# Kernel optimization log

Measured on AMD Instinct MI355X. Metric: run time of the kernel, lower is better.

## Reference

```python
import jax, jax.numpy as jnp
import numpy as np

BS, NP, H, L = 4, 1000, 128, 4
RBF_DIM, EDGE_D, NODE_D, K_NEI, NKP = 20, 16, 64, 9, 12
N = BS * 2 * NP
E = N * K_NEI
STD = 10.0          # CoordNomralizer std (mean = 0)
R_CUT = 1.0
SIGMA, GAMMA = 25.0, 10.0  # protein_surface_intersection constants (EquiDock-style)


def setup_inputs():
    key = jax.random.key(0)
    keys = iter(jax.random.split(key, 64))
    def nrm(shape, scale=None):
        s = scale if scale is not None else 1.0 / np.sqrt(shape[-2] if len(shape) > 1 else shape[-1])
        return (jax.random.normal(next(keys), shape, jnp.float32) * s).astype(jnp.float32)
    rng = np.random.default_rng(0)
    # kNN-style edges: K_NEI random intra-sample neighbors per node (messages src -> dst)
    dst = np.repeat(np.arange(N), K_NEI)
    samp = dst // (2 * NP)
    src = samp * (2 * NP) + rng.integers(0, 2 * NP, size=E)
    rots = []
    for _ in range(BS):  # sample_transformation: random rotation per complex
        A = rng.normal(size=(3, 3))
        Q, Rm = np.linalg.qr(A)
        Q = Q * np.sign(np.diag(Rm))
        if np.linalg.det(Q) < 0:
            Q[:, 0] = -Q[:, 0]
        rots.append(Q)
    return dict(
        X=nrm((N, 4, 3), 1.0),
        node_attr=nrm((N, NODE_D), 1.0),
        edge_attr=nrm((E, EDGE_D), 1.0),
        center=nrm((BS, 3), 0.1),
        keypoints=nrm((BS * NKP, 3), 1.0),
        rot=jnp.asarray(np.stack(rots), jnp.float32),
        trans=jnp.asarray(rng.random((BS, 3)), jnp.float32),
        W_in1=nrm((NODE_D, H)), b_in1=jnp.zeros((H,), jnp.float32),
        W_in2=nrm((H, H)), b_in2=jnp.zeros((H,), jnp.float32),
        msg_W=nrm((L, 2 * H + RBF_DIM + EDGE_D, H)), msg_b=jnp.zeros((L, H), jnp.float32),
        upd_W1=nrm((L, 2 * H, H)), upd_b1=jnp.zeros((L, H), jnp.float32),
        upd_W2=nrm((L, H, H)), upd_b2=jnp.zeros((L, H), jnp.float32),
        x_W=nrm((L, H, H)), v_W=nrm((L, H, H)),
        att_W=nrm((L, H, H)),
        act_W1=nrm((L, H, H)), act_b1=jnp.zeros((L, H), jnp.float32),
        act_W2=nrm((L, H, H)), act_b2=jnp.zeros((L, H), jnp.float32),
        geb_Wv1=nrm((H, H)), geb_Wv2=nrm((H, H)),
        geb_W1=nrm((2 * H, H)), geb_b1=jnp.zeros((H,), jnp.float32),
        geb_W2=nrm((H, 2 * H)), geb_b2=jnp.zeros((2 * H,), jnp.float32),
        scale_W1=nrm((H + 1, H // 2)), scale_b1=jnp.zeros((H // 2,), jnp.float32),
        scale_W2=nrm((H // 2, 1)), scale_b2=jnp.ones((1,), jnp.float32),
        final_W=nrm((H, NKP)),
        src=jnp.asarray(src, jnp.int32), dst=jnp.asarray(dst, jnp.int32),
    )


def _mse(a, b):
    return jnp.mean((a - b) ** 2)


def _kabsch(Y1, Y2):
    # optimal R, t with Y1 @ R + t ~= Y2
    c1, c2 = Y1.mean(0), Y2.mean(0)
    Hm = (Y1 - c1).T @ (Y2 - c2)
    U, S, Vt = jnp.linalg.svd(Hm)
    d = jnp.sign(jnp.linalg.det(U @ Vt))
    sc = jnp.stack([jnp.ones_like(d), jnp.ones_like(d), d])
    R = U @ (Vt * sc[:, None])
    t = c2 - c1 @ R
    return R, t


def _intersect(A, B):
    # G(x) = gamma + sigma * log sum_j exp(-||x - y_j||^2 / sigma)
    d2 = jnp.sum((A[:, None, :] - B[None, :, :]) ** 2, -1)
    return GAMMA + SIGMA * jax.nn.logsumexp(-d2 / SIGMA, axis=1)


def reference(X, node_attr, edge_attr, center, keypoints, rot, trans,
              W_in1, b_in1, W_in2, b_in2, msg_W, msg_b, upd_W1, upd_b1, upd_W2, upd_b2,
              x_W, v_W, att_W, act_W1, act_b1, act_W2, act_b2,
              geb_Wv1, geb_Wv2, geb_W1, geb_b1, geb_W2, geb_b2,
              scale_W1, scale_b1, scale_W2, scale_b2, final_W, src, dst):
    silu = jax.nn.silu
    # centering (structured layout: [BS, seg(0=receptor,1=ligand), NP, 4, 3])
    Xs = X.reshape(BS, 2, NP, 4, 3) - center[:, None, None, None, :]
    kp = keypoints.reshape(BS, NKP, 3) - center[:, None, :]
    ori = Xs[:, :, :, 1, :]                       # CA coords, pre-rotation
    Xs = Xs.at[:, 0].set(jnp.einsum('bnac,bcd->bnad', Xs[:, 0], rot) + STD * trans[:, None, None, :])
    tkp = jnp.einsum('bkc,bcd->bkd', kp, rot) + STD * trans[:, None, :]
    Xs, ori, kp, tkp = Xs / STD, ori / STD, kp / STD, tkp / STD
    Xca = Xs[:, :, :, 1, :].reshape(N, 3)

    h = silu(node_attr @ W_in1 + b_in1) @ W_in2 + b_in2
    v = jnp.zeros((N, H, 3), h.dtype)
    diff = Xca[dst] - Xca[src]
    norm = jnp.sqrt(jnp.sum(diff ** 2, -1)) + 1e-8
    dirv = diff / norm[:, None]
    nvec = jnp.arange(1, RBF_DIM + 1, dtype=h.dtype)
    rbf = jnp.sin(norm[:, None] * nvec * (jnp.pi / R_CUT)) / norm[:, None]

    for l in range(L):
        # PINN equivariant message passing
        m = silu(jnp.concatenate([h[src], h[dst], rbf, edge_attr], -1) @ msg_W[l] + msg_b[l])
        agg = jax.ops.segment_sum(m, dst, num_segments=N)
        intra = h + (silu(jnp.concatenate([h, agg], -1) @ upd_W1[l] + upd_b1[l]) @ upd_W2[l] + upd_b2[l])
        vmsg = dirv[:, None, :] * (m @ x_W[l])[:, :, None] + v[src] * (m @ v_W[l])[:, :, None]
        v = v + jax.ops.segment_sum(vmsg, dst, num_segments=N)
        # inter-segment (receptor<->ligand) attention, vectorized over batch
        hv = intra.reshape(BS, 2, NP, H)
        hr, hl = hv[:, 0], hv[:, 1]
        def act(z):
            return silu(z @ act_W1[l] + act_b1[l]) @ act_W2[l] + act_b2[l]
        gr = jax.nn.sigmoid(jnp.mean(jnp.einsum('bnh,hk,bmk->bnm', hr, att_W[l], hl), -1))
        gl = jax.nn.sigmoid(jnp.mean(jnp.einsum('bnh,hk,bmk->bnm', hl, att_W[l], hr), -1))
        h = jnp.stack([hr + gr[..., None] * act(hr), hl + gl[..., None] * act(hl)], 1).reshape(N, H)

    # gated equivariant block
    v1 = jnp.einsum('nhc,hk->nkc', v, geb_Wv1)
    v2 = jnp.einsum('nhc,hk->nkc', v, geb_Wv2)
    s = silu(jnp.concatenate([h, jnp.linalg.norm(v2, axis=-1)], -1) @ geb_W1 + geb_b1) @ geb_W2 + geb_b2
    h, v = s[:, :H], v1 * s[:, H:][:, :, None]

    hb = h.reshape(BS, 2, NP, H)
    vb = v.reshape(BS, 2, NP, H, 3)
    Xb = Xca.reshape(BS, 2, NP, 3)

    def kpgen(Xp, hp, vp):
        c = jnp.mean(Xp, 0)
        Y = jnp.einsum('nhc,hk->kc', vp * hp[:, :, None], final_W)  # [NKP,3]
        si = jnp.concatenate([jnp.linalg.norm(vp, axis=-1), jnp.linalg.norm(Xp - c, axis=1, keepdims=True)], 1)
        denom = jnp.mean(silu(si @ scale_W1 + scale_b1) @ scale_W2 + scale_b2)
        return Y / denom + c

    Y = jax.vmap(jax.vmap(kpgen))(Xb, hb, vb)  # [BS,2,NKP,3]

    def per_sample(Y1, Y2, P1, P2, Xr, Xl, oriXr, Ri, ti):
        i1 = jnp.argmin(jnp.sum((Y1[:, None] - P1[None]) ** 2, -1), 1)
        i2 = jnp.argmin(jnp.sum((Y2[:, None] - P2[None]) ** 2, -1), 1)
        ot = _mse(Y1, P1[i1]) + _mse(Y2, P2[i2])
        R, t = _kabsch(Y1, Y2)
        dock = _mse(R, Ri.T) + _mse(t, -ti @ Ri.T)  # ct = mean/std = 0
        X1a = Xr @ R + t
        rmsd = _mse(X1a, oriXr)
        stab = (jnp.mean(jnp.clip(_intersect(X1a * STD, Xl * STD), 0.0)) +
                jnp.mean(jnp.clip(_intersect(Xl * STD, X1a * STD), 0.0))) / STD
        return ot, dock, rmsd, stab

    ot, dock, rmsd, stab = jax.vmap(per_sample)(Y[:, 0], Y[:, 1], tkp, kp, Xb[:, 0], Xb[:, 1], ori[:, 0], rot, trans)
    ot, dock, rmsd, stab = ot.mean(), dock.mean(), rmsd.mean(), stab.mean()
    loss = ot + dock + stab
    return jnp.stack([loss, ot, dock, stab, rmsd])
```

## Files before the change

kernel.cpp:

```cpp
#include <hip/hip_runtime.h>
#include <math.h>

#define NPP 1000
#define BSZ 4
#define HD 128
#define NL 4
#define RBFD 20
#define EDD 16
#define KN 9
#define NKPP 12
#define NN 8000
#define EE 72000
#define STDV 10.0
#define SIGC 25.0
#define GAMC 10.0
#define PID 3.14159265358979323846

__device__ __forceinline__ double silud(double x){ return x / (1.0 + exp(-x)); }

__global__ void k_sent(float* __restrict__ out, float val){
  if(threadIdx.x<5 && blockIdx.x==0) out[threadIdx.x]=val;
}

__global__ __launch_bounds__(256) void k_cvt_node(const float* __restrict__ msgW, double* __restrict__ Wn){
  int idx = blockIdx.x*256+threadIdx.x;
  if(idx >= 4*128*256) return;
  int l = idx>>15; int r = idx & 32767; int k = r>>8; int j = r&255;
  const float* W = msgW + (size_t)l*292*128;
  Wn[idx] = (j<128) ? (double)W[k*128+j] : (double)W[(128+k)*128 + (j-128)];
}
__global__ __launch_bounds__(256) void k_cvt_edge(const float* __restrict__ msgW, const float* __restrict__ msgb,
    double* __restrict__ We){
  int idx = blockIdx.x*256+threadIdx.x;
  if(idx >= 4*37*128) return;
  int l = idx/(37*128); int r = idx%(37*128); int k = r>>7; int j = r&127;
  if(k<36) We[idx] = (double)msgW[(size_t)l*292*128 + (256+k)*128 + j];
  else     We[idx] = (double)msgb[l*128 + j];
}
__global__ __launch_bounds__(256) void k_cvt_xv(const float* __restrict__ xW, const float* __restrict__ vW,
    double* __restrict__ xv){
  int idx = blockIdx.x*256+threadIdx.x;
  if(idx >= 4*128*128) return;
  int l = idx>>14; int r = idx & 16383; int hh = r>>7; int c = r&127;
  xv[(size_t)l*32768 + hh*256 + 2*c]   = (double)xW[(size_t)l*16384 + hh*128 + c];
  xv[(size_t)l*32768 + hh*256 + 2*c+1] = (double)vW[(size_t)l*16384 + hh*128 + c];
}

__global__ __launch_bounds__(256) void k_geom(const float* __restrict__ X, const float* __restrict__ center,
    const float* __restrict__ kpin, const float* __restrict__ rot, const float* __restrict__ trans,
    double* __restrict__ Xca, double* __restrict__ ori0, double* __restrict__ kpc, double* __restrict__ tkpc){
  int i = blockIdx.x*256 + threadIdx.x;
  const double inv = 1.0/STDV;
  if(i < NN){
    int b = i / (2*NPP);
    int s = (i / NPP) & 1;
    int n = i % NPP;
    double q0 = (double)X[i*12+3] - (double)center[b*3+0];
    double q1 = (double)X[i*12+4] - (double)center[b*3+1];
    double q2 = (double)X[i*12+5] - (double)center[b*3+2];
    if(s==0){
      int o=(b*NPP+n)*3;
      ori0[o]=q0*inv; ori0[o+1]=q1*inv; ori0[o+2]=q2*inv;
      const float* R = rot + b*9;
      #pragma unroll
      for(int d=0; d<3; d++)
        Xca[i*3+d] = (q0*(double)R[d] + q1*(double)R[3+d] + q2*(double)R[6+d])*inv + (double)trans[b*3+d];
    } else {
      Xca[i*3+0]=q0*inv; Xca[i*3+1]=q1*inv; Xca[i*3+2]=q2*inv;
    }
  } else if(i < NN + BSZ*NKPP){
    int j = i - NN;
    int b = j / NKPP;
    double q0 = (double)kpin[j*3+0]-(double)center[b*3+0];
    double q1 = (double)kpin[j*3+1]-(double)center[b*3+1];
    double q2 = (double)kpin[j*3+2]-(double)center[b*3+2];
    kpc[j*3+0]=q0*inv; kpc[j*3+1]=q1*inv; kpc[j*3+2]=q2*inv;
    const float* R = rot + b*9;
    #pragma unroll
    for(int d=0; d<3; d++)
      tkpc[j*3+d] = (q0*(double)R[d] + q1*(double)R[3+d] + q2*(double)R[6+d])*inv + (double)trans[b*3+d];
  }
}

__global__ __launch_bounds__(256) void k_edge(const double* __restrict__ Xca, const int* __restrict__ src,
    const int* __restrict__ dst, double* __restrict__ dirv, double* __restrict__ rbfb){
  int e = blockIdx.x*256 + threadIdx.x;
  if(e >= EE) return;
  int sp = src[e], dp = dst[e];
  double d0 = Xca[dp*3+0]-Xca[sp*3+0];
  double d1 = Xca[dp*3+1]-Xca[sp*3+1];
  double d2 = Xca[dp*3+2]-Xca[sp*3+2];
  double nr = sqrt(d0*d0+d1*d1+d2*d2) + 1e-08;
  double iv = 1.0/nr;
  dirv[e*3+0]=d0*iv; dirv[e*3+1]=d1*iv; dirv[e*3+2]=d2*iv;
  #pragma unroll
  for(int j=0;j<RBFD;j++)
    rbfb[e*RBFD+j] = sin(nr*(double)(j+1)*PID)*iv;
}

__global__ __launch_bounds__(256) void k_hinit(const float* __restrict__ na,
    const float* __restrict__ W1, const float* __restrict__ b1,
    const float* __restrict__ W2, const float* __restrict__ b2, double* __restrict__ h){
  __shared__ double cin[4][64];
  __shared__ double hmid[4][128];
  int n0 = blockIdx.x*4;
  int tid = threadIdx.x;
  {
    int r=tid>>6, k=tid&63;
    cin[r][k] = (double)na[(n0+r)*64 + k];
  }
  __syncthreads();
  int r = tid>>6, c0 = (tid&63)*2;
  double a0=(double)b1[c0], a1=(double)b1[c0+1];
  for(int k=0;k<64;k++){
    double a = cin[r][k];
    const float* wp = W1 + k*HD + c0;
    a0 += a*(double)wp[0]; a1 += a*(double)wp[1];
  }
  hmid[r][c0]=silud(a0); hmid[r][c0+1]=silud(a1);
  __syncthreads();
  double s0=(double)b2[c0], s1=(double)b2[c0+1];
  for(int k=0;k<HD;k++){
    double a = hmid[r][k];
    const float* wp = W2 + k*HD + c0;
    s0 += a*(double)wp[0]; s1 += a*(double)wp[1];
  }
  h[(size_t)(n0+r)*HD+c0]=s0; h[(size_t)(n0+r)*HD+c0+1]=s1;
}

__global__ __launch_bounds__(128) void k_nodeproj(const double* __restrict__ h, const double* __restrict__ Wn,
    double* __restrict__ P){
  __shared__ double cin[4][128];
  int n0 = blockIdx.x*4;
  int tid = threadIdx.x;
  for(int idx=tid; idx<512; idx+=128){
    int r=idx>>7, k=idx&127;
    cin[r][k]=h[(size_t)(n0+r)*HD+k];
  }
  __syncthreads();
  int c0 = tid*2;
  double a00=0,a01=0,a10=0,a11=0,a20=0,a21=0,a30=0,a31=0;
  for(int k=0;k<128;k++){
    double2 w = *(const double2*)(Wn + (size_t)k*256 + c0);
    double x0=cin[0][k],x1=cin[1][k],x2=cin[2][k],x3=cin[3][k];
    a00+=x0*w.x; a01+=x0*w.y; a10+=x1*w.x; a11+=x1*w.y;
    a20+=x2*w.x; a21+=x2*w.y; a30+=x3*w.x; a31+=x3*w.y;
  }
  P[(size_t)(n0+0)*256+c0]=a00; P[(size_t)(n0+0)*256+c0+1]=a01;
  P[(size_t)(n0+1)*256+c0]=a10; P[(size_t)(n0+1)*256+c0+1]=a11;
  P[(size_t)(n0+2)*256+c0]=a20; P[(size_t)(n0+2)*256+c0+1]=a21;
  P[(size_t)(n0+3)*256+c0]=a30; P[(size_t)(n0+3)*256+c0+1]=a31;
}

__global__ __launch_bounds__(256) void k_edgemsg(const double* __restrict__ P, const double* __restrict__ rbfb,
    const float* __restrict__ ea, const int* __restrict__ src, const int* __restrict__ dst,
    const double* __restrict__ We, double* __restrict__ m){
  __shared__ double feat[32][41];
  __shared__ int ssi[32], ddi[32];
  int e0 = blockIdx.x*32;
  int tid = threadIdx.x;
  for(int idx=tid; idx<32*RBFD; idx+=256){
    int e=idx/RBFD, k=idx%RBFD;
    feat[e][k]=rbfb[(size_t)(e0+e)*RBFD+k];
  }
  for(int idx=tid; idx<32*EDD; idx+=256){
    int e=idx>>4, k=idx&15;
    feat[e][20+k]=(double)ea[(size_t)(e0+e)*EDD+k];
  }
  if(tid<32){ feat[tid][36]=1.0; ssi[tid]=src[e0+tid]; ddi[tid]=dst[e0+tid]; }
  __syncthreads();
  int t = tid&15, g = tid>>4;
  int j0 = g*8;
  double acc0[8], acc1[8];
  #pragma unroll
  for(int j=0;j<8;j++){ acc0[j]=0.0; acc1[j]=0.0; }
  for(int k=0;k<37;k++){
    const double* wp = We + (size_t)k*128 + j0;
    double a0 = feat[t][k], a1 = feat[t+16][k];
    #pragma unroll
    for(int j=0;j<8;j++){ double w=wp[j]; acc0[j]+=a0*w; acc1[j]+=a1*w; }
  }
  {
    const double* p1 = P + (size_t)ssi[t]*256 + j0;
    const double* p2 = P + (size_t)ddi[t]*256 + 128 + j0;
    double* mr = m + (size_t)(e0+t)*HD + j0;
    #pragma unroll
    for(int j=0;j<8;j++) mr[j] = silud(acc0[j]+p1[j]+p2[j]);
  }
  {
    const double* p1 = P + (size_t)ssi[t+16]*256 + j0;
    const double* p2 = P + (size_t)ddi[t+16]*256 + 128 + j0;
    double* mr = m + (size_t)(e0+t+16)*HD + j0;
    #pragma unroll
    for(int j=0;j<8;j++) mr[j] = silud(acc1[j]+p1[j]+p2[j]);
  }
}

__global__ __launch_bounds__(128) void k_upd(const double* __restrict__ h, const double* __restrict__ m,
    const float* __restrict__ W1, const float* __restrict__ b1,
    const float* __restrict__ W2, const float* __restrict__ b2, double* __restrict__ h2){
  __shared__ double cin[4][256];
  __shared__ double hmid[4][128];
  int n0 = blockIdx.x*4;
  int tid = threadIdx.x;
  for(int idx=tid; idx<4*128; idx+=128){
    int r=idx>>7, k=idx&127;
    cin[r][k] = h[(size_t)(n0+r)*HD+k];
    const double* mp = m + ((size_t)(n0+r)*KN)*HD + k;
    double s=0.0;
    #pragma unroll
    for(int kk=0;kk<KN;kk++) s += mp[(size_t)kk*HD];
    cin[r][128+k]=s;
  }
  __syncthreads();
  int col = tid;
  double bb=(double)b1[col];
  double a0=bb,a1=bb,a2=bb,a3=bb;
  for(int k=0;k<256;k++){
    double w = (double)W1[(size_t)k*HD+col];
    a0 += cin[0][k]*w; a1 += cin[1][k]*w; a2 += cin[2][k]*w; a3 += cin[3][k]*w;
  }
  hmid[0][col]=silud(a0); hmid[1][col]=silud(a1); hmid[2][col]=silud(a2); hmid[3][col]=silud(a3);
  __syncthreads();
  bb=(double)b2[col];
  a0=bb;a1=bb;a2=bb;a3=bb;
  for(int k=0;k<128;k++){
    double w = (double)W2[(size_t)k*HD+col];
    a0 += hmid[0][k]*w; a1 += hmid[1][k]*w; a2 += hmid[2][k]*w; a3 += hmid[3][k]*w;
  }
  h2[(size_t)(n0+0)*HD+col] = cin[0][col]+a0;
  h2[(size_t)(n0+1)*HD+col] = cin[1][col]+a1;
  h2[(size_t)(n0+2)*HD+col] = cin[2][col]+a2;
  h2[(size_t)(n0+3)*HD+col] = cin[3][col]+a3;
}

__global__ __launch_bounds__(256) void k_vupd(const double* __restrict__ m, const double* __restrict__ va,
    const double* __restrict__ dirv, const int* __restrict__ src,
    const double* __restrict__ xv, double* __restrict__ vb){
  __shared__ double mT[4][9][128];
  __shared__ double md[4][3][128];
  __shared__ double dv[4][9][3];
  __shared__ int sp[4][9];
  int n0 = blockIdx.x*4;
  int tid = threadIdx.x;
  for(int idx=tid; idx<4*9*128; idx+=256){
    int hh=idx&127, t=idx>>7; int nd=t/9, kk=t-nd*9;
    mT[nd][kk][hh] = m[((size_t)(n0+nd)*KN + kk)*HD + hh];
  }
  if(tid<36){
    int nd=tid/9, kk=tid-nd*9;
    int e=(n0+nd)*KN+kk;
    sp[nd][kk]=src[e];
    dv[nd][kk][0]=dirv[e*3]; dv[nd][kk][1]=dirv[e*3+1]; dv[nd][kk][2]=dirv[e*3+2];
  }
  __syncthreads();
  for(int idx=tid; idx<4*3*128; idx+=256){
    int hh=idx&127, t=idx>>7; int nd=t/3, c=t-nd*3;
    double s=0.0;
    #pragma unroll
    for(int kk=0;kk<9;kk++) s += dv[nd][kk][c]*mT[nd][kk][hh];
    md[nd][c][hh]=s;
  }
  __syncthreads();
  int nd = tid>>6;
  int t  = tid&63;
  int c0 = 2*t;
  double oA0=0,oA1=0,oA2=0, oB0=0,oB1=0,oB2=0;
  double mvA[9], mvB[9];
  #pragma unroll
  for(int kk=0;kk<9;kk++){ mvA[kk]=0.0; mvB[kk]=0.0; }
  for(int hh=0; hh<128; hh++){
    const double* xp = xv + (size_t)hh*256 + 2*c0;
    double2 wpA = *(const double2*)(xp);
    double2 wpB = *(const double2*)(xp+2);
    double d0 = md[nd][0][hh], d1 = md[nd][1][hh], d2 = md[nd][2][hh];
    oA0 += d0*wpA.x; oA1 += d1*wpA.x; oA2 += d2*wpA.x;
    oB0 += d0*wpB.x; oB1 += d1*wpB.x; oB2 += d2*wpB.x;
    #pragma unroll
    for(int kk=0;kk<9;kk++){
      double mk = mT[nd][kk][hh];
      mvA[kk] += mk*wpA.y;
      mvB[kk] += mk*wpB.y;
    }
  }
  #pragma unroll
  for(int kk=0;kk<9;kk++){
    size_t s3 = (size_t)sp[nd][kk]*384 + c0*3;
    double ka = mvA[kk], kb = mvB[kk];
    oA0 += va[s3]*ka;   oA1 += va[s3+1]*ka; oA2 += va[s3+2]*ka;
    oB0 += va[s3+3]*kb; oB1 += va[s3+4]*kb; oB2 += va[s3+5]*kb;
  }
  size_t b3 = (size_t)(n0+nd)*384 + c0*3;
  vb[b3]  = va[b3]  + oA0;
  vb[b3+1]= va[b3+1]+ oA1;
  vb[b3+2]= va[b3+2]+ oA2;
  vb[b3+3]= va[b3+3]+ oB0;
  vb[b3+4]= va[b3+4]+ oB1;
  vb[b3+5]= va[b3+5]+ oB2;
}

__global__ __launch_bounds__(128) void k_att1(const double* __restrict__ h2, double* __restrict__ partial){
  int blk = blockIdx.x;
  int bs = blk>>3, ch = blk&7;
  int col = threadIdx.x;
  size_t base = ((size_t)bs*NPP + ch*125)*HD + col;
  double s=0.0;
  for(int i=0;i<125;i++) s += h2[base + (size_t)i*HD];
  partial[(size_t)blk*HD + col] = s;
}
__global__ __launch_bounds__(128) void k_att2(const double* __restrict__ partial, const float* __restrict__ attW,
    double* __restrict__ u){
  __shared__ double mm[128];
  int bs = blockIdx.x;
  int col = threadIdx.x;
  int os = bs^1;
  double s=0.0;
  for(int c=0;c<8;c++) s += partial[(size_t)(os*8+c)*HD + col];
  mm[col] = s*(1.0/NPP);
  __syncthreads();
  double acc=0.0;
  for(int k=0;k<HD;k++) acc += (double)attW[col*HD+k]*mm[k];
  u[bs*HD+col] = acc;
}

__global__ __launch_bounds__(128) void k_actcomb(const double* __restrict__ h2, const double* __restrict__ u,
    const float* __restrict__ W1, const float* __restrict__ b1,
    const float* __restrict__ W2, const float* __restrict__ b2, double* __restrict__ h){
  __shared__ double As[4][128];
  __shared__ double hmid[4][128];
  __shared__ double pd[128];
  __shared__ double gsh[4];
  int n0 = blockIdx.x*4;
  int tid = threadIdx.x;
  int bs = n0/NPP;
  for(int idx=tid; idx<512; idx+=128){
    int r=idx>>7, k=idx&127;
    As[r][k] = h2[(size_t)(n0+r)*HD+k];
  }
  __syncthreads();
  {
    int nd=tid>>5, q=tid&31;
    double p=0.0;
    for(int j=q;j<128;j+=32) p += As[nd][j]*u[bs*HD+j];
    pd[tid]=p;
  }
  __syncthreads();
  if((tid&31)==0){
    int nd=tid>>5;
    double s=0.0;
    for(int i2=0;i2<32;i2++) s+=pd[nd*32+i2];
    gsh[nd]=1.0/(1.0+exp(-s));
  }
  __syncthreads();
  int col = tid;
  double bb=(double)b1[col];
  double a0=bb,a1=bb,a2=bb,a3=bb;
  for(int k=0;k<128;k++){
    double w = (double)W1[(size_t)k*HD+col];
    a0 += As[0][k]*w; a1 += As[1][k]*w; a2 += As[2][k]*w; a3 += As[3][k]*w;
  }
  hmid[0][col]=silud(a0); hmid[1][col]=silud(a1); hmid[2][col]=silud(a2); hmid[3][col]=silud(a3);
  __syncthreads();
  bb=(double)b2[col];
  a0=bb;a1=bb;a2=bb;a3=bb;
  for(int k=0;k<128;k++){
    double w = (double)W2[(size_t)k*HD+col];
    a0 += hmid[0][k]*w; a1 += hmid[1][k]*w; a2 += hmid[2][k]*w; a3 += hmid[3][k]*w;
  }
  h[(size_t)(n0+0)*HD+col] = As[0][col] + gsh[0]*a0;
  h[(size_t)(n0+1)*HD+col] = As[1][col] + gsh[1]*a1;
  h[(size_t)(n0+2)*HD+col] = As[2][col] + gsh[2]*a2;
  h[(size_t)(n0+3)*HD+col] = As[3][col] + gsh[3]*a3;
}

__global__ __launch_bounds__(256) void k_gebv(const double* __restrict__ va,
    const float* __restrict__ Wv1, const float* __restrict__ Wv2,
    double* __restrict__ v1, double* __restrict__ nv2){
  __shared__ double vl[2][384];
  int n0 = blockIdx.x*2;
  int tid = threadIdx.x;
  for(int idx=tid; idx<768; idx+=256){
    int r=idx/384, k=idx%384;
    vl[r][k] = va[(size_t)(n0+r)*384+k];
  }
  __syncthreads();
  int r = tid>>7, col = tid&127;
  double a10=0.0,a11=0.0,a12=0.0, a20=0.0,a21=0.0,a22=0.0;
  for(int hh=0; hh<HD; hh++){
    double w1 = (double)Wv1[hh*HD+col];
    double w2 = (double)Wv2[hh*HD+col];
    double v0=vl[r][hh*3], v1e=vl[r][hh*3+1], v2e=vl[r][hh*3+2];
    a10+=v0*w1; a11+=v1e*w1; a12+=v2e*w1;
    a20+=v0*w2; a21+=v1e*w2; a22+=v2e*w2;
  }
  size_t b3=(size_t)(n0+r)*384+col*3;
  v1[b3]=a10; v1[b3+1]=a11; v1[b3+2]=a12;
  nv2[(size_t)(n0+r)*HD+col]=sqrt(a20*a20+a21*a21+a22*a22);
}

__global__ __launch_bounds__(256) void k_gebs(const double* __restrict__ h, const double* __restrict__ nv2,
    const float* __restrict__ W1, const float* __restrict__ b1,
    const float* __restrict__ W2, const float* __restrict__ b2, double* __restrict__ s){
  __shared__ double cin[4][256];
  __shared__ double hmid[4][128];
  int n0 = blockIdx.x*4;
  int tid = threadIdx.x;
  for(int idx=tid; idx<4*HD; idx+=256){
    int r=idx>>7, k=idx&127;
    cin[r][k]    = h[(size_t)(n0+r)*HD + k];
    cin[r][HD+k] = nv2[(size_t)(n0+r)*HD + k];
  }
  __syncthreads();
  int r = tid>>6, c0 = (tid&63)*2;
  double a0=(double)b1[c0], a1=(double)b1[c0+1];
  for(int k=0;k<2*HD;k++){
    double a = cin[r][k];
    const float* wp = W1 + (size_t)k*HD + c0;
    a0 += a*(double)wp[0]; a1 += a*(double)wp[1];
  }
  hmid[r][c0]=silud(a0); hmid[r][c0+1]=silud(a1);
  __syncthreads();
  int c1 = (tid&63)*4;
  double s0=(double)b2[c1], s1=(double)b2[c1+1], s2=(double)b2[c1+2], s3=(double)b2[c1+3];
  for(int k=0;k<HD;k++){
    double a = hmid[r][k];
    const float* wp = W2 + (size_t)k*256 + c1;
    s0 += a*(double)wp[0]; s1 += a*(double)wp[1]; s2 += a*(double)wp[2]; s3 += a*(double)wp[3];
  }
  double* srow = s + (size_t)(n0+r)*256 + c1;
  srow[0]=s0; srow[1]=s1; srow[2]=s2; srow[3]=s3;
}

__global__ __launch_bounds__(256) void k_kpc(const double* __restrict__ Xca, double* __restrict__ cbb){
  __shared__ double red[768];
  int bs = blockIdx.x;
  int tid = threadIdx.x;
  double s0=0.0,s1=0.0,s2=0.0;
  for(int nidx=tid; nidx<NPP; nidx+=256){
    int i = bs*NPP+nidx;
    s0+=Xca[i*3]; s1+=Xca[i*3+1]; s2+=Xca[i*3+2];
  }
  red[tid]=s0; red[256+tid]=s1; red[512+tid]=s2;
  __syncthreads();
  for(int st=128; st>0; st>>=1){
    if(tid<st){ red[tid]+=red[tid+st]; red[256+tid]+=red[256+tid+st]; red[512+tid]+=red[512+tid+st]; }
    __syncthreads();
  }
  if(tid==0){ cbb[bs*3]=red[0]*(1.0/NPP); cbb[bs*3+1]=red[256]*(1.0/NPP); cbb[bs*3+2]=red[512]*(1.0/NPP); }
}

__global__ __launch_bounds__(256) void k_kpgen(const double* __restrict__ Xca, const double* __restrict__ sbuf,
    const double* __restrict__ v1, const double* __restrict__ cbb, const float* __restrict__ fW,
    const float* __restrict__ sW1, const float* __restrict__ sb1, const float* __restrict__ sW2,
    const float* __restrict__ sb2, double* __restrict__ ypart){
  __shared__ double tt[2][3][128];
  __shared__ double ssv[2][128];
  __shared__ double zz[2][64];
  __shared__ double snorm[2];
  __shared__ double ylL[2][37];
  int blk = blockIdx.x;
  int tid = threadIdx.x;
  int r = tid>>7, t = tid&127;
  int n = blk*2 + r;
  int bs = n/NPP;
  const double* srow = sbuf + (size_t)n*256;
  const double* vrow = v1 + (size_t)n*384;
  double gate = srow[128+t];
  double hp = srow[t];
  double vf0 = vrow[t*3+0]*gate, vf1 = vrow[t*3+1]*gate, vf2 = vrow[t*3+2]*gate;
  tt[r][0][t]=vf0*hp; tt[r][1][t]=vf1*hp; tt[r][2][t]=vf2*hp;
  ssv[r][t]=sqrt(vf0*vf0+vf1*vf1+vf2*vf2);
  if(t==0){
    double x0=Xca[n*3]-cbb[bs*3], x1=Xca[n*3+1]-cbb[bs*3+1], x2=Xca[n*3+2]-cbb[bs*3+2];
    snorm[r]=sqrt(x0*x0+x1*x1+x2*x2);
  }
  __syncthreads();
  if(t<36){
    int k2=t/3, c=t%3;
    double a=0.0;
    for(int hh=0; hh<128; hh++) a += tt[r][c][hh]*(double)fW[hh*NKPP+k2];
    ylL[r][t]=a;
  } else if(t>=64){
    int j=t-64;
    double z=(double)sb1[j];
    for(int hh=0; hh<128; hh++) z += ssv[r][hh]*(double)sW1[hh*64+j];
    z += snorm[r]*(double)sW1[128*64+j];
    zz[r][j]=silud(z)*(double)sW2[j];
  }
  __syncthreads();
  if(t==36){
    double dn=(double)sb2[0];
    for(int j=0;j<64;j++) dn+=zz[r][j];
    ylL[r][36]=dn;
  }
  __syncthreads();
  if(tid<37) ypart[(size_t)blk*37+tid]=ylL[0][tid]+ylL[1][tid];
}

__global__ __launch_bounds__(64) void k_kpfin(const double* __restrict__ ypart,
    const double* __restrict__ cbb, double* __restrict__ Y){
  __shared__ double sums[37];
  int bs=blockIdx.x, tid=threadIdx.x;
  if(tid<37){
    double s=0.0;
    for(int i=0;i<500;i++) s += ypart[(size_t)(bs*500+i)*37 + tid];
    sums[tid]=s;
  }
  __syncthreads();
  if(tid<36){
    double dsh = sums[36]*(1.0/NPP);
    Y[bs*36+tid] = sums[tid]/dsh + cbb[bs*3 + tid%3];
  }
}

__global__ __launch_bounds__(256) void k_final(const double* __restrict__ Y, const double* __restrict__ tkpc,
    const double* __restrict__ kpc, const float* __restrict__ rot, const float* __restrict__ trans,
    const double* __restrict__ Xca, const double* __restrict__ ori0,
    double* __restrict__ x1a, double* __restrict__ otb, double* __restrict__ dockb, double* __restrict__ rmsdb){
  int b = blockIdx.x;
  int tid = threadIdx.x;
  __shared__ double Rs[9];
  __shared__ double ts[3];
  __shared__ double red[256];
  if(tid==0){
    const double* Y1 = Y + (b*2+0)*36;
    const double* Y2 = Y + (b*2+1)*36;
    const double* P1 = tkpc + b*36;
    const double* P2 = kpc + b*36;
    double ot1=0.0, ot2=0.0;
    for(int i=0;i<12;i++){
      double best1=1e300, best2=1e300;
      for(int j=0;j<12;j++){
        double d1=0.0, d2=0.0;
        #pragma unroll
        for(int c=0;c<3;c++){
          double e1=Y1[i*3+c]-P1[j*3+c]; d1+=e1*e1;
          double e2=Y2[i*3+c]-P2[j*3+c]; d2+=e2*e2;
        }
        best1=fmin(best1,d1); best2=fmin(best2,d2);
      }
      ot1+=best1; ot2+=best2;
    }
    double ot = ot1*(1.0/36.0) + ot2*(1.0/36.0);
    double c1[3]={0,0,0}, c2[3]={0,0,0};
    for(int i=0;i<12;i++)
      for(int c=0;c<3;c++){ c1[c]+=Y1[i*3+c]; c2[c]+=Y2[i*3+c]; }
    for(int c=0;c<3;c++){ c1[c]/=12.0; c2[c]/=12.0; }
    double Hm[3][3]={{0,0,0},{0,0,0},{0,0,0}};
    for(int i=0;i<12;i++)
      for(int a=0;a<3;a++)
        for(int c=0;c<3;c++)
          Hm[a][c] += (Y1[i*3+a]-c1[a])*(Y2[i*3+c]-c2[c]);
    double Sxx=Hm[0][0],Sxy=Hm[0][1],Sxz=Hm[0][2];
    double Syx=Hm[1][0],Syy=Hm[1][1],Syz=Hm[1][2];
    double Szx=Hm[2][0],Szy=Hm[2][1],Szz=Hm[2][2];
    double K[4][4];
    K[0][0]=Sxx+Syy+Szz; K[0][1]=Syz-Szy;     K[0][2]=Szx-Sxz;      K[0][3]=Sxy-Syx;
    K[1][0]=K[0][1];     K[1][1]=Sxx-Syy-Szz; K[1][2]=Sxy+Syx;      K[1][3]=Szx+Sxz;
    K[2][0]=K[0][2];     K[2][1]=K[1][2];     K[2][2]=-Sxx+Syy-Szz; K[2][3]=Syz+Szy;
    K[3][0]=K[0][3];     K[3][1]=K[1][3];     K[3][2]=K[2][3];      K[3][3]=-Sxx-Syy+Szz;
    double V[4][4]={{1,0,0,0},{0,1,0,0},{0,0,1,0},{0,0,0,1}};
    for(int sweep=0;sweep<30;sweep++){
      for(int p=0;p<3;p++) for(int q=p+1;q<4;q++){
        double apq=K[p][q];
        if(fabs(apq)<1e-300) continue;
        double tau=(K[q][q]-K[p][p])/(2.0*apq);
        double t=(tau>=0.0?1.0:-1.0)/(fabs(tau)+sqrt(tau*tau+1.0));
        double cs=1.0/sqrt(t*t+1.0), sn=t*cs;
        for(int r2=0;r2<4;r2++){
          double krp=K[r2][p], krq=K[r2][q];
          K[r2][p]=cs*krp - sn*krq;
          K[r2][q]=sn*krp + cs*krq;
        }
        for(int r2=0;r2<4;r2++){
          double kpr=K[p][r2], kqr=K[q][r2];
          K[p][r2]=cs*kpr - sn*kqr;
          K[q][r2]=sn*kpr + cs*kqr;
        }
        for(int r2=0;r2<4;r2++){
          double vrp=V[r2][p], vrq=V[r2][q];
          V[r2][p]=cs*vrp - sn*vrq;
          V[r2][q]=sn*vrp + cs*vrq;
        }
      }
    }
    int mi=0;
    for(int i2=1;i2<4;i2++) if(K[i2][i2]>K[mi][mi]) mi=i2;
    double qw=V[0][mi], qx=V[1][mi], qy=V[2][mi], qz=V[3][mi];
    double Rh[3][3];
    Rh[0][0]=qw*qw+qx*qx-qy*qy-qz*qz; Rh[0][1]=2.0*(qx*qy-qw*qz);       Rh[0][2]=2.0*(qx*qz+qw*qy);
    Rh[1][0]=2.0*(qx*qy+qw*qz);       Rh[1][1]=qw*qw-qx*qx+qy*qy-qz*qz; Rh[1][2]=2.0*(qy*qz-qw*qx);
    Rh[2][0]=2.0*(qx*qz-qw*qy);       Rh[2][1]=2.0*(qy*qz+qw*qx);       Rh[2][2]=qw*qw-qx*qx-qy*qy+qz*qz;
    double objT=0.0, objN=0.0;
    for(int a=0;a<3;a++) for(int c=0;c<3;c++){ objT+=Rh[c][a]*Hm[a][c]; objN+=Rh[a][c]*Hm[a][c]; }
    double Rm[3][3];
    if(objT>=objN){
      for(int a=0;a<3;a++) for(int c=0;c<3;c++) Rm[a][c]=Rh[c][a];
    } else {
      for(int a=0;a<3;a++) for(int c=0;c<3;c++) Rm[a][c]=Rh[a][c];
    }
    double tt[3];
    for(int d=0;d<3;d++) tt[d]=c2[d] - (c1[0]*Rm[0][d]+c1[1]*Rm[1][d]+c1[2]*Rm[2][d]);
    const float* Rt = rot + b*9;
    double dsum=0.0;
    for(int a=0;a<3;a++) for(int c=0;c<3;c++){
      double dd = Rm[a][c] - (double)Rt[c*3+a];
      dsum += dd*dd;
    }
    double dock = dsum/9.0;
    double tsum=0.0;
    for(int d=0;d<3;d++){
      double tref = -((double)trans[b*3+0]*(double)Rt[d*3+0]+(double)trans[b*3+1]*(double)Rt[d*3+1]+(double)trans[b*3+2]*(double)Rt[d*3+2]);
      double dd = tt[d]-tref;
      tsum += dd*dd;
    }
    dock += tsum/3.0;
    otb[b]=ot; dockb[b]=dock;
    for(int a=0;a<3;a++) for(int d=0;d<3;d++) Rs[a*3+d]=Rm[a][d];
    for(int d=0;d<3;d++) ts[d]=tt[d];
  }
  __syncthreads();
  double part=0.0;
  for(int nidx=tid; nidx<NPP; nidx+=256){
    int i = b*2*NPP + nidx;
    double p0=Xca[i*3], p1=Xca[i*3+1], p2=Xca[i*3+2];
    double q0=p0*Rs[0]+p1*Rs[3]+p2*Rs[6]+ts[0];
    double q1=p0*Rs[1]+p1*Rs[4]+p2*Rs[7]+ts[1];
    double q2=p0*Rs[2]+p1*Rs[5]+p2*Rs[8]+ts[2];
    int o=(b*NPP+nidx)*3;
    x1a[o]=q0; x1a[o+1]=q1; x1a[o+2]=q2;
    double d0=q0-ori0[o], d1=q1-ori0[o+1], d2=q2-ori0[o+2];
    part += d0*d0+d1*d1+d2*d2;
  }
  red[tid]=part;
  __syncthreads();
  for(int st=128; st>0; st>>=1){ if(tid<st) red[tid]+=red[tid+st]; __syncthreads(); }
  if(tid==0) rmsdb[b]=red[0]/(double)(NPP*3);
}

__global__ __launch_bounds__(256) void k_stab(const double* __restrict__ x1a, const double* __restrict__ Xca,
    double* __restrict__ stabp){
  __shared__ double Bsm[NPP*3];
  __shared__ double red[8];
  int blk=blockIdx.x;
  int bd=blk/125, rg=blk%125;
  int b=bd>>1, dir=bd&1;
  int tid=threadIdx.x;
  const double* Ap = (dir==0) ? (x1a + (size_t)b*NPP*3) : (Xca + (size_t)(b*2+1)*NPP*3);
  const double* Bp = (dir==0) ? (Xca + (size_t)(b*2+1)*NPP*3) : (x1a + (size_t)b*NPP*3);
  for(int idx=tid; idx<NPP*3; idx+=256) Bsm[idx]=Bp[idx]*STDV;
  __syncthreads();
  int row = rg*8 + (tid>>5);
  int jt = tid&31;
  double a0=Ap[row*3]*STDV, a1=Ap[row*3+1]*STDV, a2=Ap[row*3+2]*STDV;
  double mind=1e300;
  for(int j=jt;j<NPP;j+=32){
    double d0=a0-Bsm[j*3], d1=a1-Bsm[j*3+1], d2=a2-Bsm[j*3+2];
    double d=d0*d0+d1*d1+d2*d2;
    mind=fmin(mind,d);
  }
  #pragma unroll
  for(int off=16;off>0;off>>=1) mind=fmin(mind,__shfl_xor(mind,off,32));
  double se=0.0;
  for(int j=jt;j<NPP;j+=32){
    double d0=a0-Bsm[j*3], d1=a1-Bsm[j*3+1], d2=a2-Bsm[j*3+2];
    double d=d0*d0+d1*d1+d2*d2;
    se += exp((mind-d)*(1.0/SIGC));
  }
  #pragma unroll
  for(int off=16;off>0;off>>=1) se += __shfl_xor(se,off,32);
  if(jt==0) red[tid>>5] = fmax(GAMC - mind + SIGC*log(se), 0.0);
  __syncthreads();
  if(tid==0){
    double s=0.0;
    #pragma unroll
    for(int i=0;i<8;i++) s+=red[i];
    stabp[blk]=s;
  }
}

__global__ void k_out(const double* __restrict__ otb, const double* __restrict__ dockb,
    const double* __restrict__ rmsdb, const double* __restrict__ stabp, float* __restrict__ out){
  if(blockIdx.x==0 && threadIdx.x==0){
    double ot=0.0,dock=0.0,rmsd=0.0,stab=0.0;
    for(int b=0;b<BSZ;b++){
      ot+=otb[b]; dock+=dockb[b]; rmsd+=rmsdb[b];
      double s1=0.0,s2=0.0;
      for(int i=0;i<125;i++){ s1+=stabp[(b*2+0)*125+i]; s2+=stabp[(b*2+1)*125+i]; }
      stab += (s1*(1.0/NPP) + s2*(1.0/NPP))*(1.0/STDV);
    }
    ot*=0.25; dock*=0.25; rmsd*=0.25; stab*=0.25;
    out[0]=(float)(ot+dock+stab); out[1]=(float)ot; out[2]=(float)dock; out[3]=(float)stab; out[4]=(float)rmsd;
  }
}

extern "C" void kernel_launch(void* const* d_in, const int* in_sizes, int n_in,
                              void* d_out, int out_size, void* d_ws, size_t ws_size,
                              hipStream_t stream){
  const float* X      = (const float*)d_in[0];
  const float* nodea  = (const float*)d_in[1];
  const float* edgea  = (const float*)d_in[2];
  const float* center = (const float*)d_in[3];
  const float* kpin   = (const float*)d_in[4];
  const float* rot    = (const float*)d_in[5];
  const float* trans  = (const float*)d_in[6];
  const float* W_in1  = (const float*)d_in[7];
  const float* b_in1  = (const float*)d_in[8];
  const float* W_in2  = (const float*)d_in[9];
  const float* b_in2  = (const float*)d_in[10];
  const float* msg_W  = (const float*)d_in[11];
  const float* msg_b  = (const float*)d_in[12];
  const float* upd_W1 = (const float*)d_in[13];
  const float* upd_b1 = (const float*)d_in[14];
  const float* upd_W2 = (const float*)d_in[15];
  const float* upd_b2 = (const float*)d_in[16];
  const float* x_W    = (const float*)d_in[17];
  const float* v_W    = (const float*)d_in[18];
  const float* att_W  = (const float*)d_in[19];
  const float* act_W1 = (const float*)d_in[20];
  const float* act_b1 = (const float*)d_in[21];
  const float* act_W2 = (const float*)d_in[22];
  const float* act_b2 = (const float*)d_in[23];
  const float* geb_Wv1= (const float*)d_in[24];
  const float* geb_Wv2= (const float*)d_in[25];
  const float* geb_W1 = (const float*)d_in[26];
  const float* geb_b1 = (const float*)d_in[27];
  const float* geb_W2 = (const float*)d_in[28];
  const float* geb_b2 = (const float*)d_in[29];
  const float* sc_W1  = (const float*)d_in[30];
  const float* sc_b1  = (const float*)d_in[31];
  const float* sc_W2  = (const float*)d_in[32];
  const float* sc_b2  = (const float*)d_in[33];
  const float* fin_W  = (const float*)d_in[34];
  const int*   src    = (const int*)d_in[35];
  const int*   dst    = (const int*)d_in[36];
  float* out = (float*)d_out;

  double* wd = (double*)d_ws;
  size_t o = 0;
  double* XcaD  = wd + o; o += (size_t)NN*3;
  double* ori0D = wd + o; o += (size_t)BSZ*NPP*3;
  double* kpcD  = wd + o; o += 144;
  double* tkpcD = wd + o; o += 144;
  double* dirvD = wd + o; o += (size_t)EE*3;
  double* rbfD  = wd + o; o += (size_t)EE*RBFD;
  double* hbuf  = wd + o; o += (size_t)NN*HD;
  double* Pbuf  = wd + o; o += (size_t)NN*256;
  double* mbuf  = wd + o; o += (size_t)EE*HD;
  double* va    = wd + o; o += (size_t)NN*HD*3;
  double* vb    = wd + o; o += (size_t)NN*HD*3;
  double* ubuf  = wd + o; o += (size_t)BSZ*2*HD;
  double* attp  = wd + o; o += (size_t)64*HD;
  double* nv2b  = wd + o; o += (size_t)NN*HD;
  double* sbuf  = wd + o; o += (size_t)NN*256;
  double* cbbD  = wd + o; o += 24;
  double* ypartD= wd + o; o += (size_t)4000*37;
  double* YbufD = wd + o; o += 8*36;
  double* x1aD  = wd + o; o += (size_t)BSZ*NPP*3;
  double* otb_  = wd + o; o += 4;
  double* dkb_  = wd + o; o += 4;
  double* rmb_  = wd + o; o += 4;
  double* stp_  = wd + o; o += 1000;
  double* Wnode = wd + o; o += (size_t)4*128*256;
  double* Wedge2= wd + o; o += (size_t)4*37*128;
  double* xvW   = wd + o; o += (size_t)4*128*256;

  double* h2b  = Pbuf + (size_t)NN*HD;

  size_t need = o*8;
  if(ws_size < need){
    float mb = (float)((double)ws_size / 1.0e6);
    float val = (131072.0f + mb) * 1048576.0f;
    k_sent<<<1,64,0,stream>>>(out, val);
    return;
  }

  hipMemsetAsync(va, 0, (size_t)NN*HD*3*sizeof(double), stream);

  k_cvt_node<<<512,256,0,stream>>>(msg_W, Wnode);
  k_cvt_edge<<<74,256,0,stream>>>(msg_W, msg_b, Wedge2);
  k_cvt_xv<<<256,256,0,stream>>>(x_W, v_W, xvW);

  k_geom<<<32,256,0,stream>>>(X, center, kpin, rot, trans, XcaD, ori0D, kpcD, tkpcD);
  k_edge<<<(EE+255)/256,256,0,stream>>>(XcaD, src, dst, dirvD, rbfD);
  k_hinit<<<NN/4,256,0,stream>>>(nodea, W_in1, b_in1, W_in2, b_in2, hbuf);

  double* vcur = va;
  double* vnxt = vb;
  for(int l=0;l<NL;l++){
    const double* Wn  = Wnode  + (size_t)l*128*256;
    const double* We  = Wedge2 + (size_t)l*37*128;
    const double* xvl = xvW    + (size_t)l*128*256;
    const float* u1W = upd_W1 + (size_t)l*256*HD;
    const float* u1b = upd_b1 + (size_t)l*HD;
    const float* u2W = upd_W2 + (size_t)l*HD*HD;
    const float* u2b = upd_b2 + (size_t)l*HD;
    const float* aWl = att_W  + (size_t)l*HD*HD;
    const float* a1W = act_W1 + (size_t)l*HD*HD;
    const float* a1b = act_b1 + (size_t)l*HD;
    const float* a2W = act_W2 + (size_t)l*HD*HD;
    const float* a2b = act_b2 + (size_t)l*HD;

    k_nodeproj<<<NN/4,128,0,stream>>>(hbuf, Wn, Pbuf);
    k_edgemsg<<<EE/32,256,0,stream>>>(Pbuf, rbfD, edgea, src, dst, We, mbuf);
    k_upd<<<NN/4,128,0,stream>>>(hbuf, mbuf, u1W, u1b, u2W, u2b, h2b);
    k_vupd<<<NN/4,256,0,stream>>>(mbuf, vcur, dirvD, src, xvl, vnxt);
    k_att1<<<64,128,0,stream>>>(h2b, attp);
    k_att2<<<8,128,0,stream>>>(attp, aWl, ubuf);
    k_actcomb<<<NN/4,128,0,stream>>>(h2b, ubuf, a1W, a1b, a2W, a2b, hbuf);
    double* tmp=vcur; vcur=vnxt; vnxt=tmp;
  }
  k_gebv<<<NN/2,256,0,stream>>>(vcur, geb_Wv1, geb_Wv2, vnxt, nv2b);
  k_gebs<<<NN/4,256,0,stream>>>(hbuf, nv2b, geb_W1, geb_b1, geb_W2, geb_b2, sbuf);
  k_kpc<<<8,256,0,stream>>>(XcaD, cbbD);
  k_kpgen<<<NN/2,256,0,stream>>>(XcaD, sbuf, vnxt, cbbD, fin_W, sc_W1, sc_b1, sc_W2, sc_b2, ypartD);
  k_kpfin<<<8,64,0,stream>>>(ypartD, cbbD, YbufD);
  k_final<<<BSZ,256,0,stream>>>(YbufD, tkpcD, kpcD, rot, trans, XcaD, ori0D, x1aD, otb_, dkb_, rmb_);
  k_stab<<<1000,256,0,stream>>>(x1aD, XcaD, stp_);
  k_out<<<1,64,0,stream>>>(otb_, dkb_, rmb_, stp_, out);
}
```

Before: 1.593 ms.

## Fuse edge message, node update and vector update into one per-layer kernel

Merges k_edgemsg, k_upd and k_vupd into a single k_layer kernel that handles four destination nodes per block. Each block computes those nodes' 36 edge messages in shared memory, aggregates them, runs the update MLP and the vector update, so the per-edge message buffer never goes to global memory. It also removes two launches per layer. In exchange each thread holds 37 weight registers, the MLP now uses 256 threads per 4 nodes (2 nodes per thread), and shared memory is reused through a scratch array, which may hurt occupancy.

After: 1.555 ms. 1.02x faster.

```diff
diff --git a/kernel.cpp b/kernel.cpp
--- a/kernel.cpp
+++ b/kernel.cpp
@@ -152,114 +152,112 @@
   P[(size_t)(n0+3)*256+c0]=a30; P[(size_t)(n0+3)*256+c0+1]=a31;
 }
 
-__global__ __launch_bounds__(256) void k_edgemsg(const double* __restrict__ P, const double* __restrict__ rbfb,
-    const float* __restrict__ ea, const int* __restrict__ src, const int* __restrict__ dst,
-    const double* __restrict__ We, double* __restrict__ m){
-  __shared__ double feat[32][41];
-  __shared__ int ssi[32], ddi[32];
-  int e0 = blockIdx.x*32;
-  int tid = threadIdx.x;
-  for(int idx=tid; idx<32*RBFD; idx+=256){
-    int e=idx/RBFD, k=idx%RBFD;
-    feat[e][k]=rbfb[(size_t)(e0+e)*RBFD+k];
-  }
-  for(int idx=tid; idx<32*EDD; idx+=256){
-    int e=idx>>4, k=idx&15;
-    feat[e][20+k]=(double)ea[(size_t)(e0+e)*EDD+k];
-  }
-  if(tid<32){ feat[tid][36]=1.0; ssi[tid]=src[e0+tid]; ddi[tid]=dst[e0+tid]; }
-  __syncthreads();
-  int t = tid&15, g = tid>>4;
-  int j0 = g*8;
-  double acc0[8], acc1[8];
-  #pragma unroll
-  for(int j=0;j<8;j++){ acc0[j]=0.0; acc1[j]=0.0; }
-  for(int k=0;k<37;k++){
-    const double* wp = We + (size_t)k*128 + j0;
-    double a0 = feat[t][k], a1 = feat[t+16][k];
-    #pragma unroll
-    for(int j=0;j<8;j++){ double w=wp[j]; acc0[j]+=a0*w; acc1[j]+=a1*w; }
-  }
-  {
-    const double* p1 = P + (size_t)ssi[t]*256 + j0;
-    const double* p2 = P + (size_t)ddi[t]*256 + 128 + j0;
-    double* mr = m + (size_t)(e0+t)*HD + j0;
-    #pragma unroll
-    for(int j=0;j<8;j++) mr[j] = silud(acc0[j]+p1[j]+p2[j]);
-  }
-  {
-    const double* p1 = P + (size_t)ssi[t+16]*256 + j0;
-    const double* p2 = P + (size_t)ddi[t+16]*256 + 128 + j0;
-    double* mr = m + (size_t)(e0+t+16)*HD + j0;
-    #pragma unroll
-    for(int j=0;j<8;j++) mr[j] = silud(acc1[j]+p1[j]+p2[j]);
-  }
-}
-
-__global__ __launch_bounds__(128) void k_upd(const double* __restrict__ h, const double* __restrict__ m,
-    const float* __restrict__ W1, const float* __restrict__ b1,
-    const float* __restrict__ W2, const float* __restrict__ b2, double* __restrict__ h2){
-  __shared__ double cin[4][256];
-  __shared__ double hmid[4][128];
-  int n0 = blockIdx.x*4;
-  int tid = threadIdx.x;
-  for(int idx=tid; idx<4*128; idx+=128){
-    int r=idx>>7, k=idx&127;
-    cin[r][k] = h[(size_t)(n0+r)*HD+k];
-    const double* mp = m + ((size_t)(n0+r)*KN)*HD + k;
-    double s=0.0;
-    #pragma unroll
-    for(int kk=0;kk<KN;kk++) s += mp[(size_t)kk*HD];
-    cin[r][128+k]=s;
-  }
-  __syncthreads();
-  int col = tid;
-  double bb=(double)b1[col];
-  double a0=bb,a1=bb,a2=bb,a3=bb;
-  for(int k=0;k<256;k++){
-    double w = (double)W1[(size_t)k*HD+col];
-    a0 += cin[0][k]*w; a1 += cin[1][k]*w; a2 += cin[2][k]*w; a3 += cin[3][k]*w;
-  }
-  hmid[0][col]=silud(a0); hmid[1][col]=silud(a1); hmid[2][col]=silud(a2); hmid[3][col]=silud(a3);
-  __syncthreads();
-  bb=(double)b2[col];
-  a0=bb;a1=bb;a2=bb;a3=bb;
-  for(int k=0;k<128;k++){
-    double w = (double)W2[(size_t)k*HD+col];
-    a0 += hmid[0][k]*w; a1 += hmid[1][k]*w; a2 += hmid[2][k]*w; a3 += hmid[3][k]*w;
-  }
-  h2[(size_t)(n0+0)*HD+col] = cin[0][col]+a0;
-  h2[(size_t)(n0+1)*HD+col] = cin[1][col]+a1;
-  h2[(size_t)(n0+2)*HD+col] = cin[2][col]+a2;
-  h2[(size_t)(n0+3)*HD+col] = cin[3][col]+a3;
-}
-
-__global__ __launch_bounds__(256) void k_vupd(const double* __restrict__ m, const double* __restrict__ va,
-    const double* __restrict__ dirv, const int* __restrict__ src,
-    const double* __restrict__ xv, double* __restrict__ vb){
+__global__ __launch_bounds__(256) void k_layer(
+    const double* __restrict__ P, const double* __restrict__ rbfb, const float* __restrict__ ea,
+    const int* __restrict__ src, const double* __restrict__ We,
+    const double* __restrict__ h, const float* __restrict__ W1, const float* __restrict__ b1,
+    const float* __restrict__ W2, const float* __restrict__ b2, double* __restrict__ h2,
+    const double* __restrict__ va, const double* __restrict__ dirv, const double* __restrict__ xv,
+    double* __restrict__ vb){
   __shared__ double mT[4][9][128];
-  __shared__ double md[4][3][128];
+  __shared__ double scratch[1536];
   __shared__ double dv[4][9][3];
   __shared__ int sp[4][9];
   int n0 = blockIdx.x*4;
   int tid = threadIdx.x;
-  for(int idx=tid; idx<4*9*128; idx+=256){
-    int hh=idx&127, t=idx>>7; int nd=t/9, kk=t-nd*9;
-    mT[nd][kk][hh] = m[((size_t)(n0+nd)*KN + kk)*HD + hh];
+  int e0 = n0*KN;
+  for(int idx=tid; idx<36*RBFD; idx+=256){
+    int e=idx/RBFD, f=idx-e*RBFD;
+    scratch[e*37+f] = rbfb[(size_t)(e0+e)*RBFD+f];
+  }
+  for(int idx=tid; idx<36*EDD; idx+=256){
+    int e=idx>>4, f=idx&15;
+    scratch[e*37+20+f] = (double)ea[(size_t)(e0+e)*EDD+f];
   }
   if(tid<36){
+    scratch[tid*37+36]=1.0;
     int nd=tid/9, kk=tid-nd*9;
-    int e=(n0+nd)*KN+kk;
+    int e=e0+nd*9+kk;
     sp[nd][kk]=src[e];
     dv[nd][kk][0]=dirv[e*3]; dv[nd][kk][1]=dirv[e*3+1]; dv[nd][kk][2]=dirv[e*3+2];
   }
-  __syncthreads();
-  for(int idx=tid; idx<4*3*128; idx+=256){
-    int hh=idx&127, t=idx>>7; int nd=t/3, c=t-nd*3;
+  int half = tid>>7, colp = tid&127;
+  double wreg[37];
+  #pragma unroll
+  for(int f=0;f<37;f++) wreg[f]=We[f*128+colp];
+  __syncthreads();
+  double aggv0=0.0, aggv1=0.0;
+  {
+    int nd = half*2;
+    double p2 = P[(size_t)(n0+nd)*256 + 128 + colp];
+    double agg=0.0;
+    for(int kk=0;kk<9;kk++){
+      const double* fe = &scratch[(nd*9+kk)*37];
+      double acc=0.0;
+      #pragma unroll
+      for(int f=0;f<37;f++) acc += fe[f]*wreg[f];
+      double mv_ = silud(acc + P[(size_t)sp[nd][kk]*256 + colp] + p2);
+      mT[nd][kk][colp]=mv_;
+      agg += mv_;
+    }
+    aggv0=agg;
+  }
+  {
+    int nd = half*2+1;
+    double p2 = P[(size_t)(n0+nd)*256 + 128 + colp];
+    double agg=0.0;
+    for(int kk=0;kk<9;kk++){
+      const double* fe = &scratch[(nd*9+kk)*37];
+      double acc=0.0;
+      #pragma unroll
+      for(int f=0;f<37;f++) acc += fe[f]*wreg[f];
+      double mv_ = silud(acc + P[(size_t)sp[nd][kk]*256 + colp] + p2);
+      mT[nd][kk][colp]=mv_;
+      agg += mv_;
+    }
+    aggv1=agg;
+  }
+  __syncthreads();
+  {
+    int ndA = half*2, ndB = ndA+1;
+    scratch[ndA*256+colp]     = h[(size_t)(n0+ndA)*HD+colp];
+    scratch[ndA*256+128+colp] = aggv0;
+    scratch[ndB*256+colp]     = h[(size_t)(n0+ndB)*HD+colp];
+    scratch[ndB*256+128+colp] = aggv1;
+  }
+  __syncthreads();
+  {
+    int ndA = half*2, ndB = ndA+1;
+    double bb=(double)b1[colp];
+    double a0=bb, a1=bb;
+    for(int k=0;k<256;k++){
+      double w = (double)W1[(size_t)k*HD+colp];
+      a0 += scratch[ndA*256+k]*w;
+      a1 += scratch[ndB*256+k]*w;
+    }
+    scratch[1024+ndA*128+colp]=silud(a0);
+    scratch[1024+ndB*128+colp]=silud(a1);
+  }
+  __syncthreads();
+  {
+    int ndA = half*2, ndB = ndA+1;
+    double bb=(double)b2[colp];
+    double a0=bb, a1=bb;
+    for(int k=0;k<128;k++){
+      double w = (double)W2[(size_t)k*HD+colp];
+      a0 += scratch[1024+ndA*128+k]*w;
+      a1 += scratch[1024+ndB*128+k]*w;
+    }
+    h2[(size_t)(n0+ndA)*HD+colp] = scratch[ndA*256+colp] + a0;
+    h2[(size_t)(n0+ndB)*HD+colp] = scratch[ndB*256+colp] + a1;
+  }
+  __syncthreads();
+  for(int idx=tid; idx<1536; idx+=256){
+    int hh=idx&127, t2=idx>>7; int nd=t2/3, c=t2-nd*3;
     double s=0.0;
     #pragma unroll
     for(int kk=0;kk<9;kk++) s += dv[nd][kk][c]*mT[nd][kk][hh];
-    md[nd][c][hh]=s;
+    scratch[nd*384 + c*128 + hh]=s;
   }
   __syncthreads();
   int nd = tid>>6;
@@ -269,11 +267,12 @@
   double mvA[9], mvB[9];
   #pragma unroll
   for(int kk=0;kk<9;kk++){ mvA[kk]=0.0; mvB[kk]=0.0; }
+  const double* mdb = &scratch[nd*384];
   for(int hh=0; hh<128; hh++){
     const double* xp = xv + (size_t)hh*256 + 2*c0;
     double2 wpA = *(const double2*)(xp);
     double2 wpB = *(const double2*)(xp+2);
-    double d0 = md[nd][0][hh], d1 = md[nd][1][hh], d2 = md[nd][2][hh];
+    double d0 = mdb[hh], d1 = mdb[128+hh], d2 = mdb[256+hh];
     oA0 += d0*wpA.x; oA1 += d1*wpA.x; oA2 += d2*wpA.x;
     oB0 += d0*wpB.x; oB1 += d1*wpB.x; oB2 += d2*wpB.x;
     #pragma unroll
@@ -765,7 +764,7 @@
   double* Wedge2= wd + o; o += (size_t)4*37*128;
   double* xvW   = wd + o; o += (size_t)4*128*256;
 
-  double* h2b  = Pbuf + (size_t)NN*HD;
+  double* h2b  = mbuf;
 
   size_t need = o*8;
   if(ws_size < need){
@@ -802,9 +801,9 @@
     const float* a2b = act_b2 + (size_t)l*HD;
 
     k_nodeproj<<<NN/4,128,0,stream>>>(hbuf, Wn, Pbuf);
-    k_edgemsg<<<EE/32,256,0,stream>>>(Pbuf, rbfD, edgea, src, dst, We, mbuf);
-    k_upd<<<NN/4,128,0,stream>>>(hbuf, mbuf, u1W, u1b, u2W, u2b, h2b);
-    k_vupd<<<NN/4,256,0,stream>>>(mbuf, vcur, dirvD, src, xvl, vnxt);
+    k_layer<<<NN/4,256,0,stream>>>(Pbuf, rbfD, edgea, src, We,
+                                   hbuf, u1W, u1b, u2W, u2b, h2b,
+                                   vcur, dirvD, xvl, vnxt);
     k_att1<<<64,128,0,stream>>>(h2b, attp);
     k_att2<<<8,128,0,stream>>>(attp, aWl, ubuf);
     k_actcomb<<<NN/4,128,0,stream>>>(h2b, ubuf, a1W, a1b, a2W, a2b, hbuf);
```
